# Kernel tuning notes

Measured on AMD Instinct MI355X. Metric: run time of the kernel, lower is better.

## Reference

```python
import jax, jax.numpy as jnp
import numpy as np

B, L, H, N, NL = 2, 160000, 128, 64, 4
TS, MR, CLS, LMAX = 1001, 16, 88, 1024
REP = TS * MR  # 16016


def setup_inputs() -> dict:
    key = jax.random.key(0)
    ks = jax.random.split(key, 16)
    def g(k, shape, s=0.02):
        return jax.random.normal(k, shape, jnp.float32) * s
    return {
        "x": jax.random.normal(ks[0], (B, L), jnp.float32),
        "enc_w": g(ks[1], (1, H), 1.0),
        "enc_b": g(ks[2], (H,)),
        "log_dt": jax.random.uniform(ks[3], (NL, H), jnp.float32, float(np.log(1e-3)), float(np.log(1e-1))),
        "log_A_real": jnp.log(0.5 * jnp.ones((NL, H, N), jnp.float32)),
        "A_imag": jnp.tile((np.pi * np.arange(N, dtype=np.float32))[None, None, :], (NL, H, 1)),
        "C_re": g(ks[4], (NL, H, N), 0.5 ** 0.5),
        "C_im": g(ks[5], (NL, H, N), 0.5 ** 0.5),
        "D": g(ks[6], (NL, H), 1.0),
        "out_w": g(ks[7], (NL, 2 * H, H), H ** -0.5),
        "out_b": g(ks[8], (NL, 2 * H)),
        "ln_g": jnp.ones((NL, H), jnp.float32),
        "ln_b": jnp.zeros((NL, H), jnp.float32),
        "dec_w": g(ks[9], (H, REP), H ** -0.5),
        "dec_b": g(ks[10], (REP,)),
        "head_w": g(ks[11], (4, MR, CLS), MR ** -0.5),
        "head_b": g(ks[12], (4, CLS)),
    }


def _s4_layer(u, log_dt, log_A_real, A_imag, C_re, C_im, D, out_w, out_b):
    # u: (B, H, L). S4D-style diagonal SSM kernel of length LMAX + FFT causal conv.
    dt = jnp.exp(log_dt)                         # (H,)
    A = -jnp.exp(log_A_real) + 1j * A_imag       # (H, N)
    C = C_re + 1j * C_im                         # (H, N)
    dtA = A * dt[:, None]                        # (H, N)
    Ct = C * (jnp.exp(dtA) - 1.0) / A            # ZOH-ish discretization
    l = jnp.arange(LMAX)
    vand = jnp.exp(dtA[:, :, None] * l)          # (H, N, LMAX) Vandermonde
    K = 2.0 * jnp.real(jnp.einsum('hn,hnl->hl', Ct, vand))  # (H, LMAX)
    n = L + LMAX                                 # linear (causal) conv via FFT
    uf = jnp.fft.rfft(u, n=n)                    # (B, H, n//2+1)
    kf = jnp.fft.rfft(K, n=n)                    # (H, n//2+1)
    y = jnp.fft.irfft(uf * kf[None], n=n)[..., :L]
    y = y + D[None, :, None] * u                 # skip connection
    y = jax.nn.gelu(y)
    # position-wise output linear H -> 2H, then GLU
    z = jnp.einsum('bhl,ph->bpl', y, out_w) + out_b[None, :, None]
    a, b = jnp.split(z, 2, axis=1)
    return a * jax.nn.sigmoid(b)


def _layernorm(v, g, b):
    # v: (B, L, H), normalize over H
    mu = v.mean(-1, keepdims=True)
    var = v.var(-1, keepdims=True)
    return (v - mu) / jnp.sqrt(var + 1e-5) * g + b


def reference(x, enc_w, enc_b, log_dt, log_A_real, A_imag, C_re, C_im, D,
              out_w, out_b, ln_g, ln_b, dec_w, dec_b, head_w, head_b):
    # encoder: (B, L, 1) -> (B, L, H)
    h = x[..., None] * enc_w[0][None, None, :] + enc_b  # (B, L, H)
    u = jnp.swapaxes(h, 1, 2)                            # (B, H, L)
    for i in range(NL):
        z = _s4_layer(u, log_dt[i], log_A_real[i], A_imag[i], C_re[i], C_im[i],
                      D[i], out_w[i], out_b[i])
        u = z + u                                        # residual
        v = _layernorm(jnp.swapaxes(u, 1, 2), ln_g[i], ln_b[i])  # post-norm
        u = jnp.swapaxes(v, 1, 2)
    feat = jnp.swapaxes(u, 1, 2).mean(axis=1)            # (B, H) mean-pool over L
    rep = feat @ dec_w + dec_b                           # (B, REP)
    rep = rep.reshape(B, TS, MR)                         # (B, 1001, 16)
    # 4 heads: [reg_onset, reg_offset, frame, velocity] stacked -> (4, B, TS, CLS)
    outs = jnp.einsum('btm,kmc->kbtc', rep, head_w) + head_b[:, None, None, :]
    return outs
```

## Files before the change

### kernel.cpp

```cpp
#include <hip/hip_runtime.h>
#include <math.h>

#define B_ 2
#define L_ 160000
#define H_ 128
#define N_ 64
#define NL_ 4
#define LMAX_ 1024
#define TS_ 1001
#define MR_ 16
#define CLS_ 88
#define REP_ 16016

#define NSUB_ 79
#define NJ_ 40
#define WIN_ 3208
#define WINS_ 3216
#define OUTB_ 2048
#define KE_STRIDE_ 1536

typedef unsigned short ushort_t;
typedef unsigned int uint_t;
typedef short bf16x8 __attribute__((ext_vector_type(8)));
typedef float f32x4 __attribute__((ext_vector_type(4)));

__device__ __forceinline__ float bf2f(ushort_t h) {
  uint_t u = ((uint_t)h) << 16;
  return __uint_as_float(u);
}
__device__ __forceinline__ ushort_t f2bf(float f) {
  uint_t u = __float_as_uint(f);
  uint_t r = (u + 0x7fffu + ((u >> 16) & 1u)) >> 16;
  return (ushort_t)r;
}

__global__ __launch_bounds__(256) void k_encode(const float* __restrict__ x,
                                                const float* __restrict__ enc_w,
                                                const float* __restrict__ enc_b,
                                                float* __restrict__ u) {
  int idx = blockIdx.x * 256 + threadIdx.x;
  int idx4 = idx * 4;
  int b = idx4 / (H_ * L_);
  int rem = idx4 - b * (H_ * L_);
  int h = rem / L_;
  int l = rem - h * L_;
  float w = enc_w[h], bb = enc_b[h];
  float4 xv = *(const float4*)(x + b * L_ + l);
  float4 o = make_float4(xv.x * w + bb, xv.y * w + bb, xv.z * w + bb, xv.w * w + bb);
  *(float4*)(u + (long long)(b * H_ + h) * L_ + l) = o;
}

__global__ __launch_bounds__(256) void k_ct(const float* __restrict__ log_dt,
                                            const float* __restrict__ log_A_real,
                                            const float* __restrict__ A_imag,
                                            const float* __restrict__ C_re,
                                            const float* __restrict__ C_im,
                                            float* __restrict__ ct,
                                            float* __restrict__ feat) {
  int idx = blockIdx.x * 256 + threadIdx.x;
  if (idx < B_ * H_) feat[idx] = 0.f;
  if (idx >= NL_ * H_ * N_) return;
  int h = (idx / N_) % H_;
  int i = idx / (N_ * H_);
  float dt = expf(log_dt[i * H_ + h]);
  float are = -expf(log_A_real[idx]);
  float aim = A_imag[idx];
  float dr = are * dt, di = aim * dt;
  float e = expf(dr);
  float si, co;
  sincosf(di, &si, &co);
  float er = e * co - 1.0f;
  float ei = e * si;
  float den = are * are + aim * aim;
  float qr = (er * are + ei * aim) / den;
  float qi = (ei * are - er * aim) / den;
  float cr = C_re[idx], cim = C_im[idx];
  double dd = (double)aim * (double)dt * 0.15915494309189535;
  dd -= floor(dd);
  uint_t P = (uint_t)(unsigned long long)(dd * 4294967296.0);
  ct[idx * 4 + 0] = dr;
  ct[idx * 4 + 1] = __uint_as_float(P);
  ct[idx * 4 + 2] = cr * qr - cim * qi;
  ct[idx * 4 + 3] = cr * qi + cim * qr;
}

__global__ __launch_bounds__(256) void k_ke(const float* __restrict__ ct,
                                            ushort_t* __restrict__ Ke) {
  int q = blockIdx.x & 3;
  int ih = blockIdx.x >> 2;
  __shared__ float4 cs[N_];
  if (threadIdx.x < N_) cs[threadIdx.x] = ((const float4*)ct)[ih * N_ + threadIdx.x];
  __syncthreads();
  for (int s = q * 384 + threadIdx.x; s < (q + 1) * 384; s += 256) {
    int d = s - 256;
    float val = 0.f;
    if (d >= 0 && d < LMAX_) {
      float fl = (float)d;
      float acc = 0.f;
      #pragma unroll 4
      for (int n = 0; n < N_; n++) {
        float4 qv = cs[n];
        float e = __expf(qv.x * fl);
        uint_t ph = __float_as_uint(qv.y) * (uint_t)d;
        float ang = (float)ph * 2.3283064365386963e-10f;
        float si = __builtin_amdgcn_sinf(ang);
        float co = __builtin_amdgcn_cosf(ang);
        acc += e * (qv.z * co - qv.w * si);
      }
      val = 2.f * acc;
    }
    Ke[(size_t)ih * KE_STRIDE_ + s] = f2bf(val);
  }
}

__global__ __launch_bounds__(256) void k_wprep(const float* __restrict__ W,
                                               ushort_t* __restrict__ Wb) {
  int idx = blockIdx.x * 256 + threadIdx.x;
  Wb[idx] = f2bf(W[idx]);
}

__global__ __launch_bounds__(256) void k_conv_mfma(const float* __restrict__ u,
                                                   const ushort_t* __restrict__ Ke,
                                                   const float* __restrict__ Dv,
                                                   ushort_t* __restrict__ y,
                                                   int layer) {
  int sub = blockIdx.x % NSUB_;
  int bh = blockIdx.x / NSUB_;
  int h = bh & (H_ - 1);
  int O0 = sub * OUTB_;
  int Gmax = O0 + 2063;
  __shared__ ushort_t win[4 * WINS_];
  __shared__ ushort_t kes[KE_STRIDE_];
  int tid = threadIdx.x;
  int lane = tid & 63, w = tid >> 6;
  int m = lane & 15, g = lane >> 4;

  {
    const ushort_t* keh0 = Ke + (size_t)(layer * H_ + h) * KE_STRIDE_;
    if (tid < KE_STRIDE_ / 8)
      *(bf16x8*)(kes + 8 * tid) = *(const bf16x8*)(keh0 + 8 * tid);
  }

  const float* ubh = u + (size_t)bh * L_;
  for (int T = tid; T < WIN_ / 8; T += 256) {
    int topt = Gmax - 8 * T;
    ushort_t vb[16];
    if (topt - 15 >= 0 && topt < L_) {
      const float4* fp = (const float4*)(ubh + topt - 15);
      float4 q0 = fp[0], q1 = fp[1], q2 = fp[2], q3 = fp[3];
      float tmp[16] = {q0.x, q0.y, q0.z, q0.w, q1.x, q1.y, q1.z, q1.w,
                       q2.x, q2.y, q2.z, q2.w, q3.x, q3.y, q3.z, q3.w};
      #pragma unroll
      for (int d = 0; d < 16; d++) vb[d] = f2bf(tmp[15 - d]);
    } else {
      #pragma unroll
      for (int d = 0; d < 16; d++) {
        int gl = topt - d;
        float v = (gl >= 0 && gl < L_) ? ubh[gl] : 0.f;
        vb[d] = f2bf(v);
      }
    }
    #pragma unroll
    for (int p = 0; p < 4; p++) {
      union { bf16x8 v; ushort_t s[8]; } gr;
      #pragma unroll
      for (int e = 0; e < 8; e++) gr.s[e] = vb[p + e];
      *(bf16x8*)((char*)win + p * (2 * WINS_) + 16 * T) = gr.v;
    }
  }
  __syncthreads();

  const char* wb = (const char*)win;
  const ushort_t* kf0 = kes + 16 * m + 8 * g;
  int l0A = O0 + (w << 9);
  f32x4 accA = {0.f, 0.f, 0.f, 0.f}, accB = {0.f, 0.f, 0.f, 0.f};
  int t0 = Gmax - l0A - m + 8 * g - 256;
  bf16x8 ring[8];
  #pragma unroll
  for (int s = -8; s < NJ_; s++) {
    int tS = t0 + (s << 5);
    int pS = tS & 3;
    const char* base = wb + pS * (2 * WINS_) + 2 * (tS - pS);
    union { bf16x8 v; short4 h[2]; } f;
    f.h[0] = *(const short4*)base;
    f.h[1] = *(const short4*)(base + 8);
    if (s >= 0)
      accA = __builtin_amdgcn_mfma_f32_16x16x32_bf16(f.v, ring[s & 7], accA, 0, 0, 0);
    if (s <= 31) {
      bf16x8 kn = *(const bf16x8*)(kf0 + 32 * (s + 8));
      accB = __builtin_amdgcn_mfma_f32_16x16x32_bf16(f.v, kn, accB, 0, 0, 0);
      ring[(s + 8) & 7] = kn;
    }
  }

  float Dh = Dv[layer * H_ + h];
  ushort_t* ybh = y + (size_t)bh * L_;
  #pragma unroll
  for (int tile = 0; tile < 2; tile++) {
    f32x4 acc = tile ? accB : accA;
    int l0 = l0A + tile * 256;
    int outb = l0 + 16 * m + 4 * g;
    int tu = Gmax - outb - 3;
    int pu = tu & 3;
    union { short4 s4; ushort_t us[4]; } uu;
    uu.s4 = *(const short4*)(wb + pu * (2 * WINS_) + 2 * (tu - pu));
    union { ushort_t s[4]; short4 v; } pk;
    #pragma unroll
    for (int r = 0; r < 4; r++) {
      float uval = bf2f(uu.us[3 - r]);
      float v = acc[r] + Dh * uval;
      float z2 = 1.5957691216057308f * (v + 0.044715f * v * v * v);
      pk.s[r] = f2bf(v / (1.f + __expf(-z2)));
    }
    if (outb < L_) *(short4*)(ybh + outb) = pk.v;
  }
}

__global__ __launch_bounds__(256) void k_fused(const ushort_t* __restrict__ y,
                                               const ushort_t* __restrict__ Wb,
                                               const float* __restrict__ ob,
                                               float* __restrict__ u,
                                               const float* __restrict__ lng,
                                               const float* __restrict__ lnb,
                                               int last,
                                               float* __restrict__ feat) {
  __shared__ ushort_t yT[64 * 136];
  __shared__ float redS[4 * 64] __attribute__((aligned(16)));
  __shared__ float redQ[4 * 64] __attribute__((aligned(16)));
  __shared__ float redM[64] __attribute__((aligned(16)));
  __shared__ float redR[64] __attribute__((aligned(16)));
  int lblk = blockIdx.x, b = blockIdx.y;
  int lc0 = lblk * 64;
  int tid = threadIdx.x;
  int lane = tid & 63, w = tid >> 6;
  int m = lane & 15, g = lane >> 4;

  bf16x8 Wf[4][4];
  #pragma unroll
  for (int pj = 0; pj < 4; pj++) {
    int pbase = (pj < 2) ? (32 * w + 16 * pj) : (128 + 32 * w + 16 * (pj - 2));
    const ushort_t* wrow = Wb + (pbase + m) * 128 + 8 * g;
    #pragma unroll
    for (int ks = 0; ks < 4; ks++)
      Wf[pj][ks] = *(const bf16x8*)(wrow + 32 * ks);
  }

  f32x4 uo[2][4];
  float oba[2], obs[2], gam[2], bet[2];
  #pragma unroll
  for (int pj = 0; pj < 2; pj++) {
    int pa = 32 * w + 16 * pj + m;
    const float* urow = u + (size_t)(b * H_ + pa) * L_ + lc0;
    #pragma unroll
    for (int lj = 0; lj < 4; lj++)
      uo[pj][lj] = *(const f32x4*)(urow + 16 * lj + 4 * g);
    oba[pj] = ob[pa];
    obs[pj] = ob[pa + 128];
    gam[pj] = lng[pa];
    bet[pj] = lnb[pa];
  }

  {
    int s = tid & 7;
    int kkb = tid >> 3;
    #pragma unroll
    for (int p = 0; p < 4; p++) {
      int kk = kkb + 32 * p;
      const ushort_t* yp = y + ((size_t)b * H_ + kk) * L_ + lc0 + 8 * s;
      uint4 vv = *(const uint4*)yp;
      const ushort_t* hp = (const ushort_t*)&vv;
      int sw = 8 * ((kk >> 3) ^ s) + (kk & 7);
      #pragma unroll
      for (int e = 0; e < 8; e++)
        yT[(8 * s + e) * 136 + sw] = hp[e];
    }
  }
  __syncthreads();

  f32x4 acc[4][4];
  #pragma unroll
  for (int pj = 0; pj < 4; pj++)
    #pragma unroll
    for (int lj = 0; lj < 4; lj++) acc[pj][lj] = (f32x4){0.f, 0.f, 0.f, 0.f};
  #pragma unroll
  for (int ks = 0; ks < 4; ks++) {
    bf16x8 yf[4];
    #pragma unroll
    for (int lj = 0; lj < 4; lj++) {
      int l = 16 * lj + m;
      yf[lj] = *(const bf16x8*)(yT + l * 136 + 8 * ((4 * ks + g) ^ (l >> 3)));
    }
    #pragma unroll
    for (int pj = 0; pj < 4; pj++)
      #pragma unroll
      for (int lj = 0; lj < 4; lj++)
        acc[pj][lj] = __builtin_amdgcn_mfma_f32_16x16x32_bf16(yf[lj], Wf[pj][ks],
                                                              acc[pj][lj], 0, 0, 0);
  }

  #pragma unroll
  for (int pj = 0; pj < 2; pj++) {
    #pragma unroll
    for (int lj = 0; lj < 4; lj++) {
      #pragma unroll
      for (int r = 0; r < 4; r++) {
        float a = acc[pj][lj][r] + oba[pj];
        float sv = acc[pj + 2][lj][r] + obs[pj];
        acc[pj][lj][r] = a * (1.f / (1.f + __expf(-sv))) + uo[pj][lj][r];
      }
    }
  }

  #pragma unroll
  for (int lj = 0; lj < 4; lj++) {
    #pragma unroll
    for (int r = 0; r < 4; r++) {
      float v0 = acc[0][lj][r], v1 = acc[1][lj][r];
      float s = v0 + v1, q = v0 * v0 + v1 * v1;
      s += __shfl_xor(s, 1);  q += __shfl_xor(q, 1);
      s += __shfl_xor(s, 2);  q += __shfl_xor(q, 2);
      s += __shfl_xor(s, 4);  q += __shfl_xor(q, 4);
      s += __shfl_xor(s, 8);  q += __shfl_xor(q, 8);
      if (m == 0) {
        int l = 16 * lj + 4 * g + r;
        redS[w * 64 + l] = s;
        redQ[w * 64 + l] = q;
      }
    }
  }
  __syncthreads();
  if (tid < 64) {
    float s = redS[tid] + redS[64 + tid] + redS[128 + tid] + redS[192 + tid];
    float q = redQ[tid] + redQ[64 + tid] + redQ[128 + tid] + redQ[192 + tid];
    float mean = s * (1.f / 128.f);
    float var = q * (1.f / 128.f) - mean * mean;
    redM[tid] = mean;
    redR[tid] = rsqrtf(var + 1e-5f);
  }
  __syncthreads();

  #pragma unroll
  for (int pj = 0; pj < 2; pj++) {
    int pa = 32 * w + 16 * pj + m;
    float* urow = u + (size_t)(b * H_ + pa) * L_ + lc0;
    float pool = 0.f;
    #pragma unroll
    for (int lj = 0; lj < 4; lj++) {
      int l0 = 16 * lj + 4 * g;
      f32x4 mn = *(const f32x4*)(redM + l0);
      f32x4 rs = *(const f32x4*)(redR + l0);
      f32x4 out;
      #pragma unroll
      for (int r = 0; r < 4; r++)
        out[r] = (acc[pj][lj][r] - mn[r]) * rs[r] * gam[pj] + bet[pj];
      if (!last) *(f32x4*)(urow + l0) = out;
      else pool += out[0] + out[1] + out[2] + out[3];
    }
    if (last) {
      pool += __shfl_xor(pool, 16);
      pool += __shfl_xor(pool, 32);
      if (g == 0) atomicAdd(&feat[b * H_ + pa], pool * (1.f / L_));
    }
  }
}

__global__ __launch_bounds__(256) void k_dec(const float* __restrict__ feat,
                                             const float* __restrict__ dw,
                                             const float* __restrict__ db,
                                             float* __restrict__ rep) {
  int idx = blockIdx.x * 256 + threadIdx.x;
  if (idx >= B_ * REP_) return;
  int b = idx / REP_, r = idx - b * REP_;
  float s = db[r];
  #pragma unroll 8
  for (int h = 0; h < H_; h++) s = fmaf(feat[b * H_ + h], dw[h * REP_ + r], s);
  rep[idx] = s;
}

__global__ __launch_bounds__(256) void k_head(const float* __restrict__ rep,
                                              const float* __restrict__ hw,
                                              const float* __restrict__ hb,
                                              float* __restrict__ out) {
  int idx = blockIdx.x * 256 + threadIdx.x;
  if (idx >= 4 * B_ * TS_ * CLS_) return;
  int c = idx % CLS_;
  int t = (idx / CLS_) % TS_;
  int b = (idx / (CLS_ * TS_)) % B_;
  int k = idx / (CLS_ * TS_ * B_);
  float s = hb[k * CLS_ + c];
  const float* rp = rep + ((long long)b * TS_ + t) * MR_;
  #pragma unroll
  for (int m = 0; m < MR_; m++) s = fmaf(rp[m], hw[(k * MR_ + m) * CLS_ + c], s);
  out[idx] = s;
}

extern "C" void kernel_launch(void* const* d_in, const int* in_sizes, int n_in,
                              void* d_out, int out_size, void* d_ws, size_t ws_size,
                              hipStream_t stream) {
  const float* x = (const float*)d_in[0];
  const float* enc_w = (const float*)d_in[1];
  const float* enc_b = (const float*)d_in[2];
  const float* log_dt = (const float*)d_in[3];
  const float* log_A_real = (const float*)d_in[4];
  const float* A_imag = (const float*)d_in[5];
  const float* C_re = (const float*)d_in[6];
  const float* C_im = (const float*)d_in[7];
  const float* Dv = (const float*)d_in[8];
  const float* out_w = (const float*)d_in[9];
  const float* out_b = (const float*)d_in[10];
  const float* ln_g = (const float*)d_in[11];
  const float* ln_b = (const float*)d_in[12];
  const float* dec_w = (const float*)d_in[13];
  const float* dec_b = (const float*)d_in[14];
  const float* head_w = (const float*)d_in[15];
  const float* head_b = (const float*)d_in[16];

  if (ws_size < 249000000ULL) return;

  float* ws = (float*)d_ws;
  float* u = ws;
  ushort_t* y = (ushort_t*)(ws + 40960000);
  ushort_t* Ke = (ushort_t*)(ws + 40960000 + 20480000);
  float* ct = ws + 40960000 + 20480000 + 393216;
  ushort_t* Wb = (ushort_t*)(ct + 131072);
  float* feat = ct + 131072 + 65536;
  float* rep = feat + 256;

  k_encode<<<(B_ * H_ * L_ / 4 + 255) / 256, 256, 0, stream>>>(x, enc_w, enc_b, u);
  k_ct<<<(NL_ * H_ * N_ + 255) / 256, 256, 0, stream>>>(log_dt, log_A_real, A_imag,
                                                        C_re, C_im, ct, feat);
  k_ke<<<NL_ * H_ * 4, 256, 0, stream>>>(ct, Ke);
  k_wprep<<<NL_ * 256 * 128 / 256, 256, 0, stream>>>(out_w, Wb);

  for (int i = 0; i < NL_; i++) {
    k_conv_mfma<<<B_ * H_ * NSUB_, 256, 0, stream>>>(u, Ke, Dv, y, i);
    k_fused<<<dim3(L_ / 64, B_), 256, 0, stream>>>(
        y, Wb + (size_t)i * 256 * 128, out_b + i * 256, u,
        ln_g + i * H_, ln_b + i * H_, (i == NL_ - 1) ? 1 : 0, feat);
  }
  k_dec<<<(B_ * REP_ + 255) / 256, 256, 0, stream>>>(feat, dec_w, dec_b, rep);
  k_head<<<(4 * B_ * TS_ * CLS_ + 255) / 256, 256, 0, stream>>>(rep, head_w, head_b,
                                                               (float*)d_out);
}
```

Before: 944.9 us.

## Store residual stream activations in bf16 instead of fp32

The residual/normalized activation buffer u is now kept in bf16 across encode, convolution window loads, and the fused GLU+layernorm kernel, which halves its memory footprint and traffic. The conv kernel no longer converts fp32 to bf16 when building its window, and the fused kernel reads and writes 2-byte values. The cost is extra rounding of the residual path at each layer, which may reduce accuracy relative to the fp32 reference.

```diff
diff --git a/kernel.cpp b/kernel.cpp
--- a/kernel.cpp
+++ b/kernel.cpp
@@ -37,17 +37,22 @@
 __global__ __launch_bounds__(256) void k_encode(const float* __restrict__ x,
                                                 const float* __restrict__ enc_w,
                                                 const float* __restrict__ enc_b,
-                                                float* __restrict__ u) {
+                                                ushort_t* __restrict__ u) {
   int idx = blockIdx.x * 256 + threadIdx.x;
-  int idx4 = idx * 4;
-  int b = idx4 / (H_ * L_);
-  int rem = idx4 - b * (H_ * L_);
+  int idx8 = idx * 8;
+  int b = idx8 / (H_ * L_);
+  int rem = idx8 - b * (H_ * L_);
   int h = rem / L_;
   int l = rem - h * L_;
   float w = enc_w[h], bb = enc_b[h];
-  float4 xv = *(const float4*)(x + b * L_ + l);
-  float4 o = make_float4(xv.x * w + bb, xv.y * w + bb, xv.z * w + bb, xv.w * w + bb);
-  *(float4*)(u + (long long)(b * H_ + h) * L_ + l) = o;
+  float4 x0 = *(const float4*)(x + b * L_ + l);
+  float4 x1 = *(const float4*)(x + b * L_ + l + 4);
+  union { ushort_t s[8]; uint4 v; } o;
+  o.s[0] = f2bf(x0.x * w + bb); o.s[1] = f2bf(x0.y * w + bb);
+  o.s[2] = f2bf(x0.z * w + bb); o.s[3] = f2bf(x0.w * w + bb);
+  o.s[4] = f2bf(x1.x * w + bb); o.s[5] = f2bf(x1.y * w + bb);
+  o.s[6] = f2bf(x1.z * w + bb); o.s[7] = f2bf(x1.w * w + bb);
+  *(uint4*)(u + (size_t)(b * H_ + h) * L_ + l) = o.v;
 }
 
 __global__ __launch_bounds__(256) void k_ct(const float* __restrict__ log_dt,
@@ -119,7 +124,7 @@
   Wb[idx] = f2bf(W[idx]);
 }
 
-__global__ __launch_bounds__(256) void k_conv_mfma(const float* __restrict__ u,
+__global__ __launch_bounds__(256) void k_conv_mfma(const ushort_t* __restrict__ u,
                                                    const ushort_t* __restrict__ Ke,
                                                    const float* __restrict__ Dv,
                                                    ushort_t* __restrict__ y,
@@ -141,23 +146,21 @@
       *(bf16x8*)(kes + 8 * tid) = *(const bf16x8*)(keh0 + 8 * tid);
   }
 
-  const float* ubh = u + (size_t)bh * L_;
+  const ushort_t* ubh = u + (size_t)bh * L_;
   for (int T = tid; T < WIN_ / 8; T += 256) {
     int topt = Gmax - 8 * T;
     ushort_t vb[16];
     if (topt - 15 >= 0 && topt < L_) {
-      const float4* fp = (const float4*)(ubh + topt - 15);
-      float4 q0 = fp[0], q1 = fp[1], q2 = fp[2], q3 = fp[3];
-      float tmp[16] = {q0.x, q0.y, q0.z, q0.w, q1.x, q1.y, q1.z, q1.w,
-                       q2.x, q2.y, q2.z, q2.w, q3.x, q3.y, q3.z, q3.w};
-      #pragma unroll
-      for (int d = 0; d < 16; d++) vb[d] = f2bf(tmp[15 - d]);
+      union { uint4 q[2]; ushort_t s[16]; } ld;
+      ld.q[0] = *(const uint4*)(ubh + topt - 15);
+      ld.q[1] = *(const uint4*)(ubh + topt - 7);
+      #pragma unroll
+      for (int d = 0; d < 16; d++) vb[d] = ld.s[15 - d];
     } else {
       #pragma unroll
       for (int d = 0; d < 16; d++) {
         int gl = topt - d;
-        float v = (gl >= 0 && gl < L_) ? ubh[gl] : 0.f;
-        vb[d] = f2bf(v);
+        vb[d] = (gl >= 0 && gl < L_) ? ubh[gl] : (ushort_t)0;
       }
     }
     #pragma unroll
@@ -219,7 +222,7 @@
 __global__ __launch_bounds__(256) void k_fused(const ushort_t* __restrict__ y,
                                                const ushort_t* __restrict__ Wb,
                                                const float* __restrict__ ob,
-                                               float* __restrict__ u,
+                                               ushort_t* __restrict__ u,
                                                const float* __restrict__ lng,
                                                const float* __restrict__ lnb,
                                                int last,
@@ -245,15 +248,15 @@
       Wf[pj][ks] = *(const bf16x8*)(wrow + 32 * ks);
   }
 
-  f32x4 uo[2][4];
+  short4 uoh[2][4];
   float oba[2], obs[2], gam[2], bet[2];
   #pragma unroll
   for (int pj = 0; pj < 2; pj++) {
     int pa = 32 * w + 16 * pj + m;
-    const float* urow = u + (size_t)(b * H_ + pa) * L_ + lc0;
+    const ushort_t* urow = u + (size_t)(b * H_ + pa) * L_ + lc0;
     #pragma unroll
     for (int lj = 0; lj < 4; lj++)
-      uo[pj][lj] = *(const f32x4*)(urow + 16 * lj + 4 * g);
+      uoh[pj][lj] = *(const short4*)(urow + 16 * lj + 4 * g);
     oba[pj] = ob[pa];
     obs[pj] = ob[pa + 128];
     gam[pj] = lng[pa];
@@ -306,7 +309,8 @@
       for (int r = 0; r < 4; r++) {
         float a = acc[pj][lj][r] + oba[pj];
         float sv = acc[pj + 2][lj][r] + obs[pj];
-        acc[pj][lj][r] = a * (1.f / (1.f + __expf(-sv))) + uo[pj][lj][r];
+        float uor = bf2f(((const ushort_t*)&uoh[pj][lj])[r]);
+        acc[pj][lj][r] = a * (1.f / (1.f + __expf(-sv))) + uor;
       }
     }
   }
@@ -342,19 +346,24 @@
   #pragma unroll
   for (int pj = 0; pj < 2; pj++) {
     int pa = 32 * w + 16 * pj + m;
-    float* urow = u + (size_t)(b * H_ + pa) * L_ + lc0;
+    ushort_t* urow = u + (size_t)(b * H_ + pa) * L_ + lc0;
     float pool = 0.f;
     #pragma unroll
     for (int lj = 0; lj < 4; lj++) {
       int l0 = 16 * lj + 4 * g;
       f32x4 mn = *(const f32x4*)(redM + l0);
       f32x4 rs = *(const f32x4*)(redR + l0);
-      f32x4 out;
-      #pragma unroll
-      for (int r = 0; r < 4; r++)
-        out[r] = (acc[pj][lj][r] - mn[r]) * rs[r] * gam[pj] + bet[pj];
-      if (!last) *(f32x4*)(urow + l0) = out;
-      else pool += out[0] + out[1] + out[2] + out[3];
+      if (!last) {
+        union { ushort_t s[4]; short4 v; } pk;
+        #pragma unroll
+        for (int r = 0; r < 4; r++)
+          pk.s[r] = f2bf((acc[pj][lj][r] - mn[r]) * rs[r] * gam[pj] + bet[pj]);
+        *(short4*)(urow + l0) = pk.v;
+      } else {
+        #pragma unroll
+        for (int r = 0; r < 4; r++)
+          pool += (acc[pj][lj][r] - mn[r]) * rs[r] * gam[pj] + bet[pj];
+      }
     }
     if (last) {
       pool += __shfl_xor(pool, 16);
@@ -415,18 +424,18 @@
   const float* head_w = (const float*)d_in[15];
   const float* head_b = (const float*)d_in[16];
 
-  if (ws_size < 249000000ULL) return;
+  if (ws_size < 167000000ULL) return;
 
   float* ws = (float*)d_ws;
-  float* u = ws;
-  ushort_t* y = (ushort_t*)(ws + 40960000);
-  ushort_t* Ke = (ushort_t*)(ws + 40960000 + 20480000);
-  float* ct = ws + 40960000 + 20480000 + 393216;
+  ushort_t* u = (ushort_t*)ws;
+  ushort_t* y = (ushort_t*)(ws + 20480000);
+  ushort_t* Ke = (ushort_t*)(ws + 20480000 + 20480000);
+  float* ct = ws + 20480000 + 20480000 + 393216;
   ushort_t* Wb = (ushort_t*)(ct + 131072);
   float* feat = ct + 131072 + 65536;
   float* rep = feat + 256;
 
-  k_encode<<<(B_ * H_ * L_ / 4 + 255) / 256, 256, 0, stream>>>(x, enc_w, enc_b, u);
+  k_encode<<<(B_ * H_ * L_ / 8 + 255) / 256, 256, 0, stream>>>(x, enc_w, enc_b, u);
   k_ct<<<(NL_ * H_ * N_ + 255) / 256, 256, 0, stream>>>(log_dt, log_A_real, A_imag,
                                                         C_re, C_im, ct, feat);
   k_ke<<<NL_ * H_ * 4, 256, 0, stream>>>(ct, Ke);
```

After: 929.7 us. About the same (-1.6%).
